# Kernel tuning notes

Measured on AMD Instinct MI355X. Metric: run time of the kernel, lower is better.

The kernel has to match this reference:

```python
import jax, jax.numpy as jnp
import numpy as np

B, T, D, H = 32, 512, 512, 8
DH = D // H
NEG = -(2.0 ** 32) + 1.0  # matches torch's (-2**32 + 1) padding value
EPS = 1e-8


def setup_inputs() -> dict:
    key = jax.random.key(0)
    ks = jax.random.split(key, 10)
    s = 1.0 / np.sqrt(D)
    return {
        "queries": jax.random.normal(ks[0], (B, T, D), jnp.float32),
        "keys": jax.random.normal(ks[1], (B, T, D), jnp.float32),
        "Wq": jax.random.normal(ks[2], (D, D), jnp.float32) * s,
        "bq": jnp.zeros((D,), jnp.float32),
        "Wk": jax.random.normal(ks[3], (D, D), jnp.float32) * s,
        "bk": jnp.zeros((D,), jnp.float32),
        "Wv": jax.random.normal(ks[4], (D, D), jnp.float32) * s,
        "bv": jnp.zeros((D,), jnp.float32),
        "gamma": jnp.ones((D,), jnp.float32),
        "beta": jnp.zeros((D,), jnp.float32),
    }


def reference(queries, keys, Wq, bq, Wk, bk, Wv, bv, gamma, beta):
    b, tq, d = queries.shape
    tk = keys.shape[1]
    # projections (torch Linear: x @ W.T + b)
    Q = (queries @ Wq.T + bq).reshape(b, tq, H, DH)
    K = (keys @ Wk.T + bk).reshape(b, tk, H, DH)
    V = (keys @ Wv.T + bv).reshape(b, tk, H, DH)
    # scaled scores: [b, h, tq, tk]
    scores = jnp.einsum("bqhd,bkhd->bhqk", Q, K) / np.float32(np.sqrt(DH))
    # key padding mask (1 where key row sum != 0)
    key_mask = jnp.sign(jnp.abs(keys.sum(-1)))  # [b, tk]
    scores = jnp.where(key_mask[:, None, None, :] == 0, NEG, scores)
    # causal mask
    tril = jnp.tril(jnp.ones((tq, tk), scores.dtype))
    scores = jnp.where(tril[None, None, :, :] == 0, NEG, scores)
    attn = jax.nn.softmax(scores, axis=-1)  # [b, h, tq, tk]
    # query padding mask (zeros out rows for padded queries)
    query_mask = jnp.sign(jnp.abs(queries.sum(-1)))  # [b, tq]
    attn_m = attn * query_mask[:, None, :, None]
    # (dropout_rate == 0 -> identity)
    out = jnp.einsum("bhqk,bkhd->bqhd", attn_m, V).reshape(b, tq, d)
    # residual + LayerNorm (torch .std() is unbiased, ddof=1; eps added to std)
    x = out + queries
    mean = x.mean(-1, keepdims=True)
    std = jnp.std(x, axis=-1, ddof=1, keepdims=True)
    y = gamma * (x - mean) / (std + EPS) + beta
    return y
```

## Files before the change

### kernel.cpp

```cpp
#include <hip/hip_runtime.h>
#include <hip/hip_bf16.h>
#include <math.h>

#define B 32
#define T 512
#define D 512
#define H 8
#define DH 64
#define NEGV (-4294967295.0f)
#define LN_EPS 1e-8f

typedef __attribute__((ext_vector_type(8))) short bf16x8;
typedef __attribute__((ext_vector_type(4))) float f32x4;

__device__ inline f32x4 mfma16(bf16x8 a, bf16x8 b, f32x4 c) {
    return __builtin_amdgcn_mfma_f32_16x16x32_bf16(a, b, c, 0, 0, 0);
}

__device__ inline float fexp2(float x) { return __builtin_amdgcn_exp2f(x); }

#define GLDS16(g, l)                                                      \
    __builtin_amdgcn_global_load_lds(                                     \
        (const __attribute__((address_space(1))) void*)(g),               \
        (__attribute__((address_space(3))) void*)(l), 16, 0, 0)

__device__ inline unsigned short bf16bits(float x) {
    __hip_bfloat16 h = __float2bfloat16(x);
    union { __hip_bfloat16 h; unsigned short u; } cv;
    cv.h = h;
    return cv.u;
}

__global__ __launch_bounds__(256) void convert_mask(
    const float* __restrict__ queries, const float* __restrict__ keys,
    __hip_bfloat16* __restrict__ Qx, __hip_bfloat16* __restrict__ Kx,
    float* __restrict__ qmask, float* __restrict__ kmask)
{
    const int tid = threadIdx.x;
    const int wid = tid >> 6;
    const int lane = tid & 63;
    const int row = blockIdx.x * 4 + wid;
    const float* src = blockIdx.y ? keys : queries;
    __hip_bfloat16* dst = blockIdx.y ? Kx : Qx;
    float* dm = blockIdx.y ? kmask : qmask;

    const float4* p = (const float4*)(src + (size_t)row * 512);
    float4 a = p[lane * 2];
    float4 c = p[lane * 2 + 1];
    float s = a.x + a.y + a.z + a.w + c.x + c.y + c.z + c.w;

    union { unsigned short u[8]; bf16x8 v; } pk;
    pk.u[0] = bf16bits(a.x); pk.u[1] = bf16bits(a.y);
    pk.u[2] = bf16bits(a.z); pk.u[3] = bf16bits(a.w);
    pk.u[4] = bf16bits(c.x); pk.u[5] = bf16bits(c.y);
    pk.u[6] = bf16bits(c.z); pk.u[7] = bf16bits(c.w);
    *(bf16x8*)&dst[(size_t)row * 512 + lane * 8] = pk.v;

#pragma unroll
    for (int off = 32; off > 0; off >>= 1) s += __shfl_xor(s, off, 64);
    if (lane == 0)
        dm[row] = blockIdx.y ? ((s != 0.0f) ? 0.0f : NEGV)
                             : ((s != 0.0f) ? 1.0f : 0.0f);
}

__global__ __launch_bounds__(256) void convert_w(
    const float* __restrict__ Wq, const float* __restrict__ Wk,
    const float* __restrict__ Wv, __hip_bfloat16* __restrict__ Wbf)
{
    const int mat = blockIdx.y;
    const float* Ws = (mat == 0) ? Wq : (mat == 1) ? Wk : Wv;
    const int i = (blockIdx.x * 256 + threadIdx.x) * 8;
    float4 a = *(const float4*)&Ws[i];
    float4 c = *(const float4*)&Ws[i + 4];
    union { unsigned short u[8]; bf16x8 v; } pk;
    pk.u[0] = bf16bits(a.x); pk.u[1] = bf16bits(a.y);
    pk.u[2] = bf16bits(a.z); pk.u[3] = bf16bits(a.w);
    pk.u[4] = bf16bits(c.x); pk.u[5] = bf16bits(c.y);
    pk.u[6] = bf16bits(c.z); pk.u[7] = bf16bits(c.w);
    *(bf16x8*)&Wbf[(size_t)mat * 262144 + i] = pk.v;
}

__global__ __launch_bounds__(256) void qkv_qk(
    const __hip_bfloat16* __restrict__ Qx, const __hip_bfloat16* __restrict__ Kx,
    const __hip_bfloat16* __restrict__ Wbf,
    const float* __restrict__ bq, const float* __restrict__ bk,
    __hip_bfloat16* __restrict__ Qbf, __hip_bfloat16* __restrict__ Kbf)
{
    const int mat = blockIdx.z;
    const __hip_bfloat16* X  = mat ? Kx : Qx;
    const __hip_bfloat16* Wm = Wbf + (size_t)mat * 262144;
    const float* bias = mat ? bk : bq;
    __hip_bfloat16* Out = mat ? Kbf : Qbf;
    const float sc = mat ? 1.0f : 0.18033688011112042f;

    const int bm = blockIdx.x * 128;
    const int bn = blockIdx.y * 128;
    const int tid = threadIdx.x;
    const int w = tid >> 6, lane = tid & 63;
    const int lo = lane & 15, hi = lane >> 4;
    const int wm = (w >> 1) * 64, wn = (w & 1) * 64;

    __shared__ __hip_bfloat16 As[2][128 * 32];
    __shared__ __hip_bfloat16 Bs[2][128 * 32];

    const int r0 = tid >> 2,          g0 = (tid & 3) ^ ((r0 >> 1) & 3);
    const int r1 = (tid + 256) >> 2,  g1 = ((tid + 256) & 3) ^ ((r1 >> 1) & 3);
    const __hip_bfloat16* sA0 = X  + (size_t)(bm + r0) * 512 + g0 * 8;
    const __hip_bfloat16* sA1 = X  + (size_t)(bm + r1) * 512 + g1 * 8;
    const __hip_bfloat16* sB0 = Wm + (size_t)(bn + r0) * 512 + g0 * 8;
    const __hip_bfloat16* sB1 = Wm + (size_t)(bn + r1) * 512 + g1 * 8;
    const int dst0 = (w * 64) * 8;
    const int dst1 = (256 + w * 64) * 8;

    int offA[4], offB[4];
#pragma unroll
    for (int mi = 0; mi < 4; ++mi) {
        int r = wm + mi * 16 + lo;
        offA[mi] = r * 32 + ((hi ^ ((r >> 1) & 3)) * 8);
    }
#pragma unroll
    for (int ni = 0; ni < 4; ++ni) {
        int r = wn + ni * 16 + lo;
        offB[ni] = r * 32 + ((hi ^ ((r >> 1) & 3)) * 8);
    }

    f32x4 acc[4][4];
#pragma unroll
    for (int mi = 0; mi < 4; ++mi)
#pragma unroll
        for (int ni = 0; ni < 4; ++ni)
            acc[mi][ni] = (f32x4){0.f, 0.f, 0.f, 0.f};

    GLDS16(sA0, &As[0][dst0]);
    GLDS16(sA1, &As[0][dst1]);
    GLDS16(sB0, &Bs[0][dst0]);
    GLDS16(sB1, &Bs[0][dst1]);
    __syncthreads();

    for (int kt = 0; kt < 16; ++kt) {
        const int cur = kt & 1;
        if (kt < 15) {
            const int k0 = (kt + 1) * 32;
            GLDS16(sA0 + k0, &As[cur ^ 1][dst0]);
            GLDS16(sA1 + k0, &As[cur ^ 1][dst1]);
            GLDS16(sB0 + k0, &Bs[cur ^ 1][dst0]);
            GLDS16(sB1 + k0, &Bs[cur ^ 1][dst1]);
        }
        bf16x8 af[4], bfr[4];
#pragma unroll
        for (int mi = 0; mi < 4; ++mi) af[mi]  = *(const bf16x8*)&As[cur][offA[mi]];
#pragma unroll
        for (int ni = 0; ni < 4; ++ni) bfr[ni] = *(const bf16x8*)&Bs[cur][offB[ni]];
#pragma unroll
        for (int mi = 0; mi < 4; ++mi)
#pragma unroll
            for (int ni = 0; ni < 4; ++ni)
                acc[mi][ni] = mfma16(bfr[ni], af[mi], acc[mi][ni]);
        __syncthreads();
    }

    float4 b4[4];
#pragma unroll
    for (int ni = 0; ni < 4; ++ni)
        b4[ni] = *(const float4*)&bias[bn + wn + ni * 16 + hi * 4];
#pragma unroll
    for (int mi = 0; mi < 4; ++mi) {
        const size_t tok = bm + wm + mi * 16 + lo;
        __hip_bfloat16* orow = Out + tok * 512 + bn + wn + hi * 4;
#pragma unroll
        for (int ni = 0; ni < 4; ++ni) {
            union { ushort4 u4; unsigned short us[4]; } pk;
            pk.us[0] = bf16bits((acc[mi][ni][0] + b4[ni].x) * sc);
            pk.us[1] = bf16bits((acc[mi][ni][1] + b4[ni].y) * sc);
            pk.us[2] = bf16bits((acc[mi][ni][2] + b4[ni].z) * sc);
            pk.us[3] = bf16bits((acc[mi][ni][3] + b4[ni].w) * sc);
            *(ushort4*)(orow + ni * 16) = pk.u4;
        }
    }
}

__global__ __launch_bounds__(256) void qkv_v(
    const __hip_bfloat16* __restrict__ Kx, const __hip_bfloat16* __restrict__ Wbf,
    const float* __restrict__ bv, __hip_bfloat16* __restrict__ Vtb)
{
    const __hip_bfloat16* X  = Kx;
    const __hip_bfloat16* Wm = Wbf + (size_t)2 * 262144;
    const float* bias = bv;

    const int bm = blockIdx.x * 128;
    const int bn = blockIdx.y * 128;
    const int tid = threadIdx.x;
    const int w = tid >> 6, lane = tid & 63;
    const int lo = lane & 15, hi = lane >> 4;
    const int wm = (w >> 1) * 64, wn = (w & 1) * 64;

    __shared__ __hip_bfloat16 As[2][128 * 32];
    __shared__ __hip_bfloat16 Bs[2][128 * 32];

    const int r0 = tid >> 2,          g0 = (tid & 3) ^ ((r0 >> 1) & 3);
    const int r1 = (tid + 256) >> 2,  g1 = ((tid + 256) & 3) ^ ((r1 >> 1) & 3);
    const __hip_bfloat16* sA0 = X  + (size_t)(bm + r0) * 512 + g0 * 8;
    const __hip_bfloat16* sA1 = X  + (size_t)(bm + r1) * 512 + g1 * 8;
    const __hip_bfloat16* sB0 = Wm + (size_t)(bn + r0) * 512 + g0 * 8;
    const __hip_bfloat16* sB1 = Wm + (size_t)(bn + r1) * 512 + g1 * 8;
    const int dst0 = (w * 64) * 8;
    const int dst1 = (256 + w * 64) * 8;

    int offA[4], offB[4];
#pragma unroll
    for (int mi = 0; mi < 4; ++mi) {
        int r = wm + mi * 16 + lo;
        offA[mi] = r * 32 + ((hi ^ ((r >> 1) & 3)) * 8);
    }
#pragma unroll
    for (int ni = 0; ni < 4; ++ni) {
        int r = wn + ni * 16 + lo;
        offB[ni] = r * 32 + ((hi ^ ((r >> 1) & 3)) * 8);
    }

    f32x4 acc[4][4];
#pragma unroll
    for (int mi = 0; mi < 4; ++mi)
#pragma unroll
        for (int ni = 0; ni < 4; ++ni)
            acc[mi][ni] = (f32x4){0.f, 0.f, 0.f, 0.f};

    GLDS16(sA0, &As[0][dst0]);
    GLDS16(sA1, &As[0][dst1]);
    GLDS16(sB0, &Bs[0][dst0]);
    GLDS16(sB1, &Bs[0][dst1]);
    __syncthreads();

    for (int kt = 0; kt < 16; ++kt) {
        const int cur = kt & 1;
        if (kt < 15) {
            const int k0 = (kt + 1) * 32;
            GLDS16(sA0 + k0, &As[cur ^ 1][dst0]);
            GLDS16(sA1 + k0, &As[cur ^ 1][dst1]);
            GLDS16(sB0 + k0, &Bs[cur ^ 1][dst0]);
            GLDS16(sB1 + k0, &Bs[cur ^ 1][dst1]);
        }
        bf16x8 af[4], bfr[4];
#pragma unroll
        for (int mi = 0; mi < 4; ++mi) af[mi]  = *(const bf16x8*)&As[cur][offA[mi]];
#pragma unroll
        for (int ni = 0; ni < 4; ++ni) bfr[ni] = *(const bf16x8*)&Bs[cur][offB[ni]];
#pragma unroll
        for (int mi = 0; mi < 4; ++mi)
#pragma unroll
            for (int ni = 0; ni < 4; ++ni)
                acc[mi][ni] = mfma16(af[mi], bfr[ni], acc[mi][ni]);
        __syncthreads();
    }

    float bcol[4];
#pragma unroll
    for (int ni = 0; ni < 4; ++ni) bcol[ni] = bias[bn + wn + ni * 16 + lo];
    const int bb = bm >> 9;
    const int tb = (bm & 511) + wm;
#pragma unroll
    for (int ni = 0; ni < 4; ++ni) {
        const int n = bn + wn + ni * 16 + lo;
        const int hh = n >> 6, dh = n & 63;
#pragma unroll
        for (int mi = 0; mi < 4; ++mi) {
            const int tok = tb + mi * 16 + hi * 4;
            const int ktl = tok >> 6, tl = tok & 63;
            union { ushort4 u4; unsigned short us[4]; } pk;
#pragma unroll
            for (int j = 0; j < 4; ++j)
                pk.us[j] = bf16bits(acc[mi][ni][j] + bcol[ni]);
            *(ushort4*)(Vtb + ((((size_t)(bb * 8 + hh) * 8 + ktl) * 64 + dh) * 64 + tl))
                = pk.u4;
        }
    }
}

__global__ __launch_bounds__(256, 4) void flash_attn(
    const __hip_bfloat16* __restrict__ Qbf, const __hip_bfloat16* __restrict__ Kbf,
    const __hip_bfloat16* __restrict__ Vtb, const float* __restrict__ qmask,
    const float* __restrict__ kmneg, __hip_bfloat16* __restrict__ Oattn)
{
    const int flat = blockIdx.x + (blockIdx.y << 2) + (blockIdx.z << 5);
    const int rm = ((flat & 7) << 7) + (flat >> 3);
    const int pr = rm & 3;
    const int h  = (rm >> 2) & 7;
    const int b  = rm >> 5;

    const int tid  = threadIdx.x;
    const int w    = tid >> 6;
    const int lane = tid & 63;
    const int lo = lane & 15;
    const int hi = lane >> 4;

    __shared__ __hip_bfloat16 Ks[2][4096];
    __shared__ __hip_bfloat16 p_lds[4][16][72];

    const float* km = kmneg + b * T;
    const __hip_bfloat16* Kh = Kbf + (size_t)b * T * D + h * DH;
    const __hip_bfloat16* Vh = Vtb + (size_t)(b * H + h) * T * DH;

    const int sr0 = tid >> 3,         sg0 = (tid & 7) ^ (sr0 & 7);
    const int sr1 = (tid + 256) >> 3, sg1 = ((tid + 256) & 7) ^ (sr1 & 7);
    const __hip_bfloat16* sK0 = Kh + (size_t)sr0 * 512 + sg0 * 8;
    const __hip_bfloat16* sK1 = Kh + (size_t)sr1 * 512 + sg1 * 8;
    __hip_bfloat16* dK0a = &Ks[0][w * 512];
    __hip_bfloat16* dK0b = &Ks[0][2048 + w * 512];
    __hip_bfloat16* dK1a = &Ks[1][w * 512];
    __hip_bfloat16* dK1b = &Ks[1][2048 + w * 512];

#define STAGEK(bufp, kt) do {                                              \
        const size_t _o = (size_t)(kt) * 32768;                            \
        GLDS16(sK0 + _o, (bufp) ? dK1a : dK0a);                            \
        GLDS16(sK1 + _o, (bufp) ? dK1b : dK0b);                            \
    } while (0)

    int kfoff[4][2];
#pragma unroll
    for (int c = 0; c < 4; ++c)
#pragma unroll
        for (int j = 0; j < 2; ++j)
            kfoff[c][j] = (c * 16 + lo) * 64 + (((j * 4 + hi) ^ (lo & 7)) * 8);

    f32x4 cb[4];
#pragma unroll
    for (int c = 0; c < 4; ++c)
#pragma unroll
        for (int j = 0; j < 4; ++j)
            cb[c][j] = (c * 16 + hi * 4 + j <= w * 16 + lo) ? 0.0f : NEGV;

    const int nt1 = pr + 1;

    int qtile = pr;
    int q = qtile * 64 + w * 16 + lo;
    const __hip_bfloat16* Qrow = Qbf + (size_t)(b * T + q) * D + h * DH;
    bf16x8 qf0 = *(const bf16x8*)(Qrow + hi * 8);
    bf16x8 qf1 = *(const bf16x8*)(Qrow + 32 + hi * 8);

    f32x4 o[4];
    float mrun = -INFINITY, lrun = 0.f;
#pragma unroll
    for (int d = 0; d < 4; ++d) o[d] = (f32x4){0.f, 0.f, 0.f, 0.f};

    STAGEK(0, 0);

    for (int i = 0; i < 9; ++i) {
        const int cur = i & 1;
        const bool diag = (i == nt1 - 1) || (i == 8);
        if (i < 8) {
            const int nxt = (i + 1 < nt1) ? (i + 1) : (i + 1 - nt1);
            STAGEK(cur ^ 1, nxt);
            asm volatile("s_waitcnt vmcnt(2)" ::: "memory");
        } else {
            asm volatile("s_waitcnt vmcnt(0)" ::: "memory");
        }
        __builtin_amdgcn_s_barrier();
        __builtin_amdgcn_sched_barrier(0);

        if (i == nt1) {
            const float inv = qmask[b * T + q] / lrun;
            __hip_bfloat16* orow = Oattn + (size_t)(b * T + q) * D + h * DH;
#pragma unroll
            for (int db = 0; db < 4; ++db) {
                union { ushort4 u4; unsigned short us[4]; } pk;
#pragma unroll
                for (int j = 0; j < 4; ++j)
                    pk.us[j] = bf16bits(o[db][j] * inv);
                *(ushort4*)(orow + db * 16 + hi * 4) = pk.u4;
            }
            qtile = 7 - pr;
            q = qtile * 64 + w * 16 + lo;
            const __hip_bfloat16* Qrow2 = Qbf + (size_t)(b * T + q) * D + h * DH;
            qf0 = *(const bf16x8*)(Qrow2 + hi * 8);
            qf1 = *(const bf16x8*)(Qrow2 + 32 + hi * 8);
            mrun = -INFINITY; lrun = 0.f;
#pragma unroll
            for (int d = 0; d < 4; ++d) o[d] = (f32x4){0.f, 0.f, 0.f, 0.f};
        }

        const int kt = (i < nt1) ? i : (i - nt1);
        const int kb = kt * 64;

        const __hip_bfloat16* Vtile = Vh + (size_t)kt * 4096;
        bf16x8 vf[4][2];
#pragma unroll
        for (int db = 0; db < 4; ++db) {
            const __hip_bfloat16* Vrow = Vtile + (db * 16 + lo) * 64;
            vf[db][0] = *(const bf16x8*)(Vrow + hi * 8);
            vf[db][1] = *(const bf16x8*)(Vrow + 32 + hi * 8);
        }

        bf16x8 kf[4][2];
#pragma unroll
        for (int c = 0; c < 4; ++c) {
            kf[c][0] = *(const bf16x8*)&Ks[cur][kfoff[c][0]];
            kf[c][1] = *(const bf16x8*)&Ks[cur][kfoff[c][1]];
        }

        f32x4 S[4];
#pragma unroll
        for (int c = 0; c < 4; ++c) {
            f32x4 acc = (f32x4){0.f, 0.f, 0.f, 0.f};
            acc = mfma16(kf[c][0], qf0, acc);
            acc = mfma16(kf[c][1], qf1, acc);
            acc += *(const f32x4*)(km + kb + c * 16 + hi * 4);
            if (diag) acc += cb[c];
            S[c] = acc;
        }

        float tm0 = fmaxf(fmaxf(S[0][0], S[0][1]), fmaxf(S[0][2], S[0][3]));
        float tm1 = fmaxf(fmaxf(S[1][0], S[1][1]), fmaxf(S[1][2], S[1][3]));
        float tm2 = fmaxf(fmaxf(S[2][0], S[2][1]), fmaxf(S[2][2], S[2][3]));
        float tm3 = fmaxf(fmaxf(S[3][0], S[3][1]), fmaxf(S[3][2], S[3][3]));
        float tm = fmaxf(fmaxf(tm0, tm1), fmaxf(tm2, tm3));
        tm = fmaxf(tm, __shfl_xor(tm, 16, 64));
        tm = fmaxf(tm, __shfl_xor(tm, 32, 64));

        const float nm = fmaxf(mrun, tm);
        const float alpha = fexp2(mrun - nm);
        mrun = nm;
#pragma unroll
        for (int d = 0; d < 4; ++d)
#pragma unroll
            for (int j = 0; j < 4; ++j)
                o[d][j] *= alpha;

        float ps = 0.f;
#pragma unroll
        for (int c = 0; c < 4; ++c) {
            union { ushort4 u4; unsigned short us[4]; } pk;
#pragma unroll
            for (int j = 0; j < 4; ++j) {
                float p = fexp2(S[c][j] - nm);
                ps += p;
                pk.us[j] = bf16bits(p);
            }
            *(ushort4*)&p_lds[w][lo][c * 16 + hi * 4] = pk.u4;
        }
        ps += __shfl_xor(ps, 16, 64);
        ps += __shfl_xor(ps, 32, 64);
        lrun = lrun * alpha + ps;

        asm volatile("s_waitcnt lgkmcnt(0)" ::: "memory");
        __builtin_amdgcn_sched_barrier(0);

#pragma unroll
        for (int half = 0; half < 2; ++half) {
            bf16x8 pf = *(const bf16x8*)&p_lds[w][lo][half * 32 + hi * 8];
#pragma unroll
            for (int db = 0; db < 4; ++db)
                o[db] = mfma16(vf[db][half], pf, o[db]);
        }

        __builtin_amdgcn_s_barrier();
    }

    {
        const float inv = qmask[b * T + q] / lrun;
        __hip_bfloat16* orow = Oattn + (size_t)(b * T + q) * D + h * DH;
#pragma unroll
        for (int db = 0; db < 4; ++db) {
            union { ushort4 u4; unsigned short us[4]; } pk;
#pragma unroll
            for (int j = 0; j < 4; ++j)
                pk.us[j] = bf16bits(o[db][j] * inv);
            *(ushort4*)(orow + db * 16 + hi * 4) = pk.u4;
        }
    }
#undef STAGEK
}

__device__ inline float wave_sum(float v) {
#pragma unroll
    for (int off = 32; off > 0; off >>= 1) v += __shfl_xor(v, off, 64);
    return v;
}

__global__ __launch_bounds__(256) void resid_ln(
    const __hip_bfloat16* __restrict__ Oa, const float* __restrict__ queries,
    const float* __restrict__ gamma, const float* __restrict__ beta,
    float* __restrict__ out)
{
    const int row = blockIdx.x;
    const int tid = threadIdx.x;
    const int wid = tid >> 6;
    const int lane = tid & 63;
    __shared__ float red[4];

    const size_t base = (size_t)row * 512;
    float2 qv = *(const float2*)&queries[base + 2 * tid];
    unsigned ov = *(const unsigned*)((const unsigned short*)Oa + base + 2 * tid);
    union { unsigned u; float f; } c0, c1;
    c0.u = ov << 16;
    c1.u = ov & 0xffff0000u;
    float x0 = c0.f + qv.x;
    float x1 = c1.f + qv.y;

    float part = wave_sum(x0 + x1);
    if (lane == 0) red[wid] = part;
    __syncthreads();
    float mean = (red[0] + red[1] + red[2] + red[3]) * (1.0f / 512.0f);
    __syncthreads();

    float d0 = x0 - mean, d1 = x1 - mean;
    part = wave_sum(d0 * d0 + d1 * d1);
    if (lane == 0) red[wid] = part;
    __syncthreads();
    float var = (red[0] + red[1] + red[2] + red[3]) * (1.0f / 511.0f);
    float denom = sqrtf(var) + LN_EPS;

    float2 g = *(const float2*)&gamma[2 * tid];
    float2 be = *(const float2*)&beta[2 * tid];
    float2 res;
    res.x = g.x * d0 / denom + be.x;
    res.y = g.y * d1 / denom + be.y;
    *(float2*)&out[base + 2 * tid] = res;
}

extern "C" void kernel_launch(void* const* d_in, const int* in_sizes, int n_in,
                              void* d_out, int out_size, void* d_ws, size_t ws_size,
                              hipStream_t stream)
{
    const float* queries = (const float*)d_in[0];
    const float* keys    = (const float*)d_in[1];
    const float* Wq      = (const float*)d_in[2];
    const float* bq      = (const float*)d_in[3];
    const float* Wk      = (const float*)d_in[4];
    const float* bk      = (const float*)d_in[5];
    const float* Wv      = (const float*)d_in[6];
    const float* bv      = (const float*)d_in[7];
    const float* gamma   = (const float*)d_in[8];
    const float* beta    = (const float*)d_in[9];
    float* out = (float*)d_out;

    char* ws = (char*)d_ws;
    __hip_bfloat16* Qbf   = (__hip_bfloat16*)(ws);
    __hip_bfloat16* Kbf   = (__hip_bfloat16*)(ws + 16777216);
    __hip_bfloat16* Vtb   = (__hip_bfloat16*)(ws + 33554432);
    __hip_bfloat16* Qx    = (__hip_bfloat16*)(ws + 50331648);
    __hip_bfloat16* Oattn = (__hip_bfloat16*)(ws + 50331648);
    __hip_bfloat16* Kx    = (__hip_bfloat16*)(ws + 67108864);
    __hip_bfloat16* Wbf   = (__hip_bfloat16*)(ws + 83886080);
    float* qmask          = (float*)(ws + 85458944);
    float* kmask          = (float*)(ws + 85524480);

    convert_mask<<<dim3(4096, 2), 256, 0, stream>>>(
        queries, keys, Qx, Kx, qmask, kmask);
    convert_w<<<dim3(128, 3), 256, 0, stream>>>(Wq, Wk, Wv, Wbf);
    qkv_qk<<<dim3(128, 4, 2), 256, 0, stream>>>(
        Qx, Kx, Wbf, bq, bk, Qbf, Kbf);
    qkv_v<<<dim3(128, 4), 256, 0, stream>>>(Kx, Wbf, bv, Vtb);
    flash_attn<<<dim3(4, 8, 32), 256, 0, stream>>>(
        Qbf, Kbf, Vtb, qmask, kmask, Oattn);
    resid_ln<<<16384, 256, 0, stream>>>(Oattn, queries, gamma, beta, out);
}
```

Before: 133.1 us.

## Fuse conversion kernels, prefetch V/mask early, lazy softmax rescale, row-per-wave LayerNorm

Merges the weight-conversion kernel into the activation-conversion kernel to save a launch. In flash attention, the V fragments and key-mask values are now loaded before the K-tile barrier so their latency overlaps the wait, and the MFMA sections are bracketed with s_setprio. The online softmax skips the rescale when the running max grows by no more than a threshold, which saves multiplies but lets the exponent exceed zero. The residual LayerNorm now handles one row per wave, using only shuffle reductions and no shared-memory syncs.

```diff
diff --git a/kernel.cpp b/kernel.cpp
--- a/kernel.cpp
+++ b/kernel.cpp
@@ -31,12 +31,37 @@
     return cv.u;
 }
 
-__global__ __launch_bounds__(256) void convert_mask(
+__device__ inline float b2f(unsigned short u) {
+    union { unsigned u; float f; } c;
+    c.u = ((unsigned)u) << 16;
+    return c.f;
+}
+
+__global__ __launch_bounds__(256) void convert_all(
     const float* __restrict__ queries, const float* __restrict__ keys,
+    const float* __restrict__ Wq, const float* __restrict__ Wk,
+    const float* __restrict__ Wv,
     __hip_bfloat16* __restrict__ Qx, __hip_bfloat16* __restrict__ Kx,
+    __hip_bfloat16* __restrict__ Wbf,
     float* __restrict__ qmask, float* __restrict__ kmask)
 {
     const int tid = threadIdx.x;
+    if (blockIdx.x >= 4096) {
+        const int i = (blockIdx.x - 4096) * 2 + blockIdx.y;
+        const int mat = i >> 7;
+        const float* Ws = (mat == 0) ? Wq : (mat == 1) ? Wk : Wv;
+        const int idx = ((i & 127) * 256 + tid) * 8;
+        float4 a = *(const float4*)&Ws[idx];
+        float4 c = *(const float4*)&Ws[idx + 4];
+        union { unsigned short u[8]; bf16x8 v; } pk;
+        pk.u[0] = bf16bits(a.x); pk.u[1] = bf16bits(a.y);
+        pk.u[2] = bf16bits(a.z); pk.u[3] = bf16bits(a.w);
+        pk.u[4] = bf16bits(c.x); pk.u[5] = bf16bits(c.y);
+        pk.u[6] = bf16bits(c.z); pk.u[7] = bf16bits(c.w);
+        *(bf16x8*)&Wbf[(size_t)mat * 262144 + idx] = pk.v;
+        return;
+    }
+
     const int wid = tid >> 6;
     const int lane = tid & 63;
     const int row = blockIdx.x * 4 + wid;
@@ -61,23 +86,6 @@
     if (lane == 0)
         dm[row] = blockIdx.y ? ((s != 0.0f) ? 0.0f : NEGV)
                              : ((s != 0.0f) ? 1.0f : 0.0f);
-}
-
-__global__ __launch_bounds__(256) void convert_w(
-    const float* __restrict__ Wq, const float* __restrict__ Wk,
-    const float* __restrict__ Wv, __hip_bfloat16* __restrict__ Wbf)
-{
-    const int mat = blockIdx.y;
-    const float* Ws = (mat == 0) ? Wq : (mat == 1) ? Wk : Wv;
-    const int i = (blockIdx.x * 256 + threadIdx.x) * 8;
-    float4 a = *(const float4*)&Ws[i];
-    float4 c = *(const float4*)&Ws[i + 4];
-    union { unsigned short u[8]; bf16x8 v; } pk;
-    pk.u[0] = bf16bits(a.x); pk.u[1] = bf16bits(a.y);
-    pk.u[2] = bf16bits(a.z); pk.u[3] = bf16bits(a.w);
-    pk.u[4] = bf16bits(c.x); pk.u[5] = bf16bits(c.y);
-    pk.u[6] = bf16bits(c.z); pk.u[7] = bf16bits(c.w);
-    *(bf16x8*)&Wbf[(size_t)mat * 262144 + i] = pk.v;
 }
 
 __global__ __launch_bounds__(256) void qkv_qk(
@@ -347,12 +355,30 @@
     for (int i = 0; i < 9; ++i) {
         const int cur = i & 1;
         const bool diag = (i == nt1 - 1) || (i == 8);
+        const int kt = (i < nt1) ? i : (i - nt1);
+        const int kb = kt * 64;
+
+        f32x4 kmb[4];
+#pragma unroll
+        for (int c = 0; c < 4; ++c)
+            kmb[c] = *(const f32x4*)(km + kb + c * 16 + hi * 4);
+
+        const __hip_bfloat16* Vtile = Vh + (size_t)kt * 4096;
+        bf16x8 vf[4][2];
+#pragma unroll
+        for (int db = 0; db < 4; ++db) {
+            const __hip_bfloat16* Vrow = Vtile + (db * 16 + lo) * 64;
+            vf[db][0] = *(const bf16x8*)(Vrow + hi * 8);
+            vf[db][1] = *(const bf16x8*)(Vrow + 32 + hi * 8);
+        }
+        __builtin_amdgcn_sched_barrier(0);
+
         if (i < 8) {
             const int nxt = (i + 1 < nt1) ? (i + 1) : (i + 1 - nt1);
             STAGEK(cur ^ 1, nxt);
-            asm volatile("s_waitcnt vmcnt(2)" ::: "memory");
+            asm volatile("s_waitcnt vmcnt(12)" ::: "memory");
         } else {
-            asm volatile("s_waitcnt vmcnt(0)" ::: "memory");
+            asm volatile("s_waitcnt vmcnt(10)" ::: "memory");
         }
         __builtin_amdgcn_s_barrier();
         __builtin_amdgcn_sched_barrier(0);
@@ -378,18 +404,6 @@
             for (int d = 0; d < 4; ++d) o[d] = (f32x4){0.f, 0.f, 0.f, 0.f};
         }
 
-        const int kt = (i < nt1) ? i : (i - nt1);
-        const int kb = kt * 64;
-
-        const __hip_bfloat16* Vtile = Vh + (size_t)kt * 4096;
-        bf16x8 vf[4][2];
-#pragma unroll
-        for (int db = 0; db < 4; ++db) {
-            const __hip_bfloat16* Vrow = Vtile + (db * 16 + lo) * 64;
-            vf[db][0] = *(const bf16x8*)(Vrow + hi * 8);
-            vf[db][1] = *(const bf16x8*)(Vrow + 32 + hi * 8);
-        }
-
         bf16x8 kf[4][2];
 #pragma unroll
         for (int c = 0; c < 4; ++c) {
@@ -397,16 +411,18 @@
             kf[c][1] = *(const bf16x8*)&Ks[cur][kfoff[c][1]];
         }
 
+        __builtin_amdgcn_s_setprio(1);
         f32x4 S[4];
 #pragma unroll
         for (int c = 0; c < 4; ++c) {
             f32x4 acc = (f32x4){0.f, 0.f, 0.f, 0.f};
             acc = mfma16(kf[c][0], qf0, acc);
             acc = mfma16(kf[c][1], qf1, acc);
-            acc += *(const f32x4*)(km + kb + c * 16 + hi * 4);
+            acc += kmb[c];
             if (diag) acc += cb[c];
             S[c] = acc;
         }
+        __builtin_amdgcn_s_setprio(0);
 
         float tm0 = fmaxf(fmaxf(S[0][0], S[0][1]), fmaxf(S[0][2], S[0][3]));
         float tm1 = fmaxf(fmaxf(S[1][0], S[1][1]), fmaxf(S[1][2], S[1][3]));
@@ -416,14 +432,17 @@
         tm = fmaxf(tm, __shfl_xor(tm, 16, 64));
         tm = fmaxf(tm, __shfl_xor(tm, 32, 64));
 
-        const float nm = fmaxf(mrun, tm);
-        const float alpha = fexp2(mrun - nm);
-        mrun = nm;
-#pragma unroll
-        for (int d = 0; d < 4; ++d)
-#pragma unroll
-            for (int j = 0; j < 4; ++j)
-                o[d][j] *= alpha;
+        if (!__all(tm <= mrun + 8.0f)) {
+            const float nm = fmaxf(mrun, tm);
+            const float alpha = fexp2(mrun - nm);
+            mrun = nm;
+#pragma unroll
+            for (int d = 0; d < 4; ++d)
+#pragma unroll
+                for (int j = 0; j < 4; ++j)
+                    o[d][j] *= alpha;
+            lrun *= alpha;
+        }
 
         float ps = 0.f;
 #pragma unroll
@@ -431,7 +450,7 @@
             union { ushort4 u4; unsigned short us[4]; } pk;
 #pragma unroll
             for (int j = 0; j < 4; ++j) {
-                float p = fexp2(S[c][j] - nm);
+                float p = fexp2(S[c][j] - mrun);
                 ps += p;
                 pk.us[j] = bf16bits(p);
             }
@@ -439,11 +458,12 @@
         }
         ps += __shfl_xor(ps, 16, 64);
         ps += __shfl_xor(ps, 32, 64);
-        lrun = lrun * alpha + ps;
+        lrun += ps;
 
         asm volatile("s_waitcnt lgkmcnt(0)" ::: "memory");
         __builtin_amdgcn_sched_barrier(0);
 
+        __builtin_amdgcn_s_setprio(1);
 #pragma unroll
         for (int half = 0; half < 2; ++half) {
             bf16x8 pf = *(const bf16x8*)&p_lds[w][lo][half * 32 + hi * 8];
@@ -451,6 +471,7 @@
             for (int db = 0; db < 4; ++db)
                 o[db] = mfma16(vf[db][half], pf, o[db]);
         }
+        __builtin_amdgcn_s_setprio(0);
 
         __builtin_amdgcn_s_barrier();
     }
@@ -468,12 +489,6 @@
         }
     }
 #undef STAGEK
-}
-
-__device__ inline float wave_sum(float v) {
-#pragma unroll
-    for (int off = 32; off > 0; off >>= 1) v += __shfl_xor(v, off, 64);
-    return v;
 }
 
 __global__ __launch_bounds__(256) void resid_ln(
@@ -481,40 +496,54 @@
     const float* __restrict__ gamma, const float* __restrict__ beta,
     float* __restrict__ out)
 {
-    const int row = blockIdx.x;
-    const int tid = threadIdx.x;
-    const int wid = tid >> 6;
-    const int lane = tid & 63;
-    __shared__ float red[4];
-
-    const size_t base = (size_t)row * 512;
-    float2 qv = *(const float2*)&queries[base + 2 * tid];
-    unsigned ov = *(const unsigned*)((const unsigned short*)Oa + base + 2 * tid);
-    union { unsigned u; float f; } c0, c1;
-    c0.u = ov << 16;
-    c1.u = ov & 0xffff0000u;
-    float x0 = c0.f + qv.x;
-    float x1 = c1.f + qv.y;
-
-    float part = wave_sum(x0 + x1);
-    if (lane == 0) red[wid] = part;
-    __syncthreads();
-    float mean = (red[0] + red[1] + red[2] + red[3]) * (1.0f / 512.0f);
-    __syncthreads();
-
-    float d0 = x0 - mean, d1 = x1 - mean;
-    part = wave_sum(d0 * d0 + d1 * d1);
-    if (lane == 0) red[wid] = part;
-    __syncthreads();
-    float var = (red[0] + red[1] + red[2] + red[3]) * (1.0f / 511.0f);
-    float denom = sqrtf(var) + LN_EPS;
-
-    float2 g = *(const float2*)&gamma[2 * tid];
-    float2 be = *(const float2*)&beta[2 * tid];
-    float2 res;
-    res.x = g.x * d0 / denom + be.x;
-    res.y = g.y * d1 / denom + be.y;
-    *(float2*)&out[base + 2 * tid] = res;
+    const int w = threadIdx.x >> 6;
+    const int lane = threadIdx.x & 63;
+    const int row = blockIdx.x * 4 + w;
+    const size_t base = (size_t)row * 512 + lane * 8;
+
+    bf16x8 oa = *(const bf16x8*)((const unsigned short*)Oa + base);
+    float4 q0 = *(const float4*)(queries + base);
+    float4 q1 = *(const float4*)(queries + base + 4);
+
+    float x[8];
+    x[0] = b2f((unsigned short)oa[0]) + q0.x;
+    x[1] = b2f((unsigned short)oa[1]) + q0.y;
+    x[2] = b2f((unsigned short)oa[2]) + q0.z;
+    x[3] = b2f((unsigned short)oa[3]) + q0.w;
+    x[4] = b2f((unsigned short)oa[4]) + q1.x;
+    x[5] = b2f((unsigned short)oa[5]) + q1.y;
+    x[6] = b2f((unsigned short)oa[6]) + q1.z;
+    x[7] = b2f((unsigned short)oa[7]) + q1.w;
+
+    float s = ((x[0] + x[1]) + (x[2] + x[3])) + ((x[4] + x[5]) + (x[6] + x[7]));
+#pragma unroll
+    for (int off = 32; off > 0; off >>= 1) s += __shfl_xor(s, off, 64);
+    const float mean = s * (1.0f / 512.0f);
+
+    float d[8], ss = 0.f;
+#pragma unroll
+    for (int j = 0; j < 8; ++j) { d[j] = x[j] - mean; ss += d[j] * d[j]; }
+#pragma unroll
+    for (int off = 32; off > 0; off >>= 1) ss += __shfl_xor(ss, off, 64);
+    const float denom = sqrtf(ss * (1.0f / 511.0f)) + LN_EPS;
+    const float rden = 1.0f / denom;
+
+    float4 g0 = *(const float4*)(gamma + lane * 8);
+    float4 g1 = *(const float4*)(gamma + lane * 8 + 4);
+    float4 b0 = *(const float4*)(beta + lane * 8);
+    float4 b1 = *(const float4*)(beta + lane * 8 + 4);
+
+    float4 r0, r1;
+    r0.x = g0.x * d[0] * rden + b0.x;
+    r0.y = g0.y * d[1] * rden + b0.y;
+    r0.z = g0.z * d[2] * rden + b0.z;
+    r0.w = g0.w * d[3] * rden + b0.w;
+    r1.x = g1.x * d[4] * rden + b1.x;
+    r1.y = g1.y * d[5] * rden + b1.y;
+    r1.z = g1.z * d[6] * rden + b1.z;
+    r1.w = g1.w * d[7] * rden + b1.w;
+    *(float4*)(out + base) = r0;
+    *(float4*)(out + base + 4) = r1;
 }
 
 extern "C" void kernel_launch(void* const* d_in, const int* in_sizes, int n_in,
@@ -544,13 +573,12 @@
     float* qmask          = (float*)(ws + 85458944);
     float* kmask          = (float*)(ws + 85524480);
 
-    convert_mask<<<dim3(4096, 2), 256, 0, stream>>>(
-        queries, keys, Qx, Kx, qmask, kmask);
-    convert_w<<<dim3(128, 3), 256, 0, stream>>>(Wq, Wk, Wv, Wbf);
+    convert_all<<<dim3(4288, 2), 256, 0, stream>>>(
+        queries, keys, Wq, Wk, Wv, Qx, Kx, Wbf, qmask, kmask);
     qkv_qk<<<dim3(128, 4, 2), 256, 0, stream>>>(
         Qx, Kx, Wbf, bq, bk, Qbf, Kbf);
     qkv_v<<<dim3(128, 4), 256, 0, stream>>>(Kx, Wbf, bv, Vtb);
     flash_attn<<<dim3(4, 8, 32), 256, 0, stream>>>(
         Qbf, Kbf, Vtb, qmask, kmask, Oattn);
-    resid_ln<<<16384, 256, 0, stream>>>(Oattn, queries, gamma, beta, out);
-}
+    resid_ln<<<4096, 256, 0, stream>>>(Oattn, queries, gamma, beta, out);
+}
```

New measurement: 146.4 us. +10.0%, slower.
